# Kernel tuning notes

Measured on AMD Instinct MI355X. Metric: run time of the kernel, lower is better.

## Reference

```python
import jax, jax.numpy as jnp
import numpy as np

B, T, C = 2, 2048, 2048
H, KV, D = 16, 4, 128
G = H // KV  # kv groups
THETA = 10000.0


def setup_inputs() -> dict:
    key = jax.random.key(0)
    ks = jax.random.split(key, 5)
    x = jax.random.normal(ks[0], (B, T, C), dtype=jnp.float32)
    wq = jax.random.normal(ks[1], (H * D, C), dtype=jnp.float32) * 0.02
    wk = jax.random.normal(ks[2], (KV * D, C), dtype=jnp.float32) * 0.02
    wv = jax.random.normal(ks[3], (KV * D, C), dtype=jnp.float32) * 0.02
    wo = jax.random.normal(ks[4], (H * D, C), dtype=jnp.float32).T * 0.02  # [C, H*D] stored as [out,in]
    wo = jnp.asarray(wo)
    # rotary frequencies: freqs_cis = exp(i * t * theta^{-2j/D}) for j in [0, D/2)
    inv_freq = 1.0 / (THETA ** (jnp.arange(0, D, 2, dtype=jnp.float32) / D))  # [D/2]
    angles = jnp.arange(T, dtype=jnp.float32)[:, None] * inv_freq[None, :]    # [T, D/2]
    freqs_cos = jnp.cos(angles)
    freqs_sin = jnp.sin(angles)
    # additive causal mask [1,1,T,T]
    mask = jnp.where(jnp.tril(jnp.ones((T, T), dtype=bool)), 0.0, -1e9).astype(jnp.float32)[None, None]
    return {"x": x, "wq": wq, "wk": wk, "wv": wv, "wo": wo,
            "freqs_cos": freqs_cos, "freqs_sin": freqs_sin, "mask": mask}


def _apply_rope(t, cos, sin):
    # t: [B, T, nH, D]; cos/sin: [T, D/2]
    th = t.reshape(*t.shape[:-1], D // 2, 2)
    t0, t1 = th[..., 0], th[..., 1]
    c = cos[None, :, None, :]
    s = sin[None, :, None, :]
    o0 = t0 * c - t1 * s
    o1 = t0 * s + t1 * c
    return jnp.stack([o0, o1], axis=-1).reshape(t.shape)


def reference(x, wq, wk, wv, wo, freqs_cos, freqs_sin, mask):
    Bx, Tx, Cx = x.shape
    xq = (x @ wq.T).reshape(Bx, Tx, H, D)
    xk = (x @ wk.T).reshape(Bx, Tx, KV, D)
    xv = (x @ wv.T).reshape(Bx, Tx, KV, D)
    xq = _apply_rope(xq, freqs_cos, freqs_sin)
    xk = _apply_rope(xk, freqs_cos, freqs_sin)
    # GQA: repeat_interleave KV heads to match query heads
    xk = jnp.repeat(xk, G, axis=2)  # [B, T, H, D]
    xv = jnp.repeat(xv, G, axis=2)
    # [B, H, T, D]
    xq = xq.transpose(0, 2, 1, 3)
    xk = xk.transpose(0, 2, 1, 3)
    xv = xv.transpose(0, 2, 1, 3)
    scores = jnp.einsum('bhqd,bhkd->bhqk', xq, xk) / jnp.sqrt(jnp.float32(D))
    scores = scores + mask
    probs = jax.nn.softmax(scores.astype(jnp.float32), axis=-1).astype(xq.dtype)
    out = jnp.einsum('bhqk,bhkd->bhqd', probs, xv)
    out = out.transpose(0, 2, 1, 3).reshape(Bx, Tx, H * D)
    return out @ wo.T
```

## Files before the change

### kernel.cpp

```cpp
#include <hip/hip_runtime.h>
#include <hip/hip_bf16.h>

typedef __bf16 bf16_t;
typedef __bf16 bf16x8 __attribute__((ext_vector_type(8)));
typedef __bf16 bf16x4 __attribute__((ext_vector_type(4)));
typedef float f32x4 __attribute__((ext_vector_type(4)));
typedef float f32x16 __attribute__((ext_vector_type(16)));

#define SCALE_Q2 0.12752518895325724f

__device__ __forceinline__ void gload_lds16(const void* g, void* l) {
  __builtin_amdgcn_global_load_lds(
      (const __attribute__((address_space(1))) void*)g,
      (__attribute__((address_space(3))) void*)l, 16, 0, 0);
}

__global__ __launch_bounds__(256) void cvt_all(
    const float* __restrict__ x, const float* __restrict__ wq,
    const float* __restrict__ wk, const float* __restrict__ wv,
    const float* __restrict__ wo, bf16_t* __restrict__ xb,
    bf16_t* __restrict__ wqkv, bf16_t* __restrict__ wo_b) {
  int i = blockIdx.x * 256 + threadIdx.x;
  const int stride = gridDim.x * 256;
  for (; i < 4718592; i += stride) {
    const int e = i * 4;
    const float* src;
    bf16_t* dst;
    if (e < 8388608) {
      src = x + e;              dst = xb + e;
    } else if (e < 12582912) {
      src = wq + (e - 8388608); dst = wqkv + (e - 8388608);
    } else if (e < 13631488) {
      src = wk + (e - 12582912); dst = wqkv + (e - 8388608);
    } else if (e < 14680064) {
      src = wv + (e - 13631488); dst = wqkv + (e - 8388608);
    } else {
      src = wo + (e - 14680064); dst = wo_b + (e - 14680064);
    }
    f32x4 v = *reinterpret_cast<const f32x4*>(src);
    bf16x4 r;
    r[0] = (bf16_t)v[0]; r[1] = (bf16_t)v[1];
    r[2] = (bf16_t)v[2]; r[3] = (bf16_t)v[3];
    *reinterpret_cast<bf16x4*>(dst) = r;
  }
}

template <typename OutT>
__global__ __launch_bounds__(256) void gemm_bt(
    const bf16_t* __restrict__ A, const bf16_t* __restrict__ W,
    OutT* __restrict__ C, int M, int N, int K) {
  __shared__ __align__(16) bf16_t As[128 * 64];
  __shared__ __align__(16) bf16_t Ws[128 * 64];
  const int tid = threadIdx.x;
  const int lane = tid & 63;
  const int wid = tid >> 6;
  const int wr = wid >> 1, wc = wid & 1;
  const int l15 = lane & 15, lg = lane >> 4;
  const int r0 = blockIdx.y * 128;
  const int c0 = blockIdx.x * 128;

  f32x4 acc[4][4];
#pragma unroll
  for (int mi = 0; mi < 4; ++mi)
#pragma unroll
    for (int ni = 0; ni < 4; ++ni)
#pragma unroll
      for (int j = 0; j < 4; ++j) acc[mi][ni][j] = 0.f;

  for (int k0 = 0; k0 < K; k0 += 64) {
#pragma unroll
    for (int s = 0; s < 4; ++s) {
      const int c = s * 256 + tid;
      const int row = c >> 3;
      const int scol = (c & 7) ^ (row & 7);
      gload_lds16(A + (size_t)(r0 + row) * K + k0 + scol * 8,
                  (char*)As + c * 16);
      gload_lds16(W + (size_t)(c0 + row) * K + k0 + scol * 8,
                  (char*)Ws + c * 16);
    }
    __syncthreads();
#pragma unroll
    for (int kk = 0; kk < 2; ++kk) {
      bf16x8 af[4], wf[4];
#pragma unroll
      for (int mi = 0; mi < 4; ++mi) {
        const int r = wr * 64 + mi * 16 + l15;
        af[mi] = *reinterpret_cast<const bf16x8*>(
            (char*)As + r * 128 + ((kk * 64 + lg * 16) ^ ((r & 7) << 4)));
      }
#pragma unroll
      for (int ni = 0; ni < 4; ++ni) {
        const int r = wc * 64 + ni * 16 + l15;
        wf[ni] = *reinterpret_cast<const bf16x8*>(
            (char*)Ws + r * 128 + ((kk * 64 + lg * 16) ^ ((r & 7) << 4)));
      }
#pragma unroll
      for (int mi = 0; mi < 4; ++mi)
#pragma unroll
        for (int ni = 0; ni < 4; ++ni)
          acc[mi][ni] = __builtin_amdgcn_mfma_f32_16x16x32_bf16(
              af[mi], wf[ni], acc[mi][ni], 0, 0, 0);
    }
    __syncthreads();
  }

#pragma unroll
  for (int mi = 0; mi < 4; ++mi)
#pragma unroll
    for (int ni = 0; ni < 4; ++ni)
#pragma unroll
      for (int j = 0; j < 4; ++j) {
        const int row = r0 + wr * 64 + mi * 16 + lg * 4 + j;
        const int col = c0 + wc * 64 + ni * 16 + l15;
        const float v = acc[mi][ni][j];
        if constexpr (__is_same(OutT, float))
          C[(size_t)row * N + col] = v;
        else
          C[(size_t)row * N + col] = (bf16_t)v;
      }
}

__global__ __launch_bounds__(256) void rope_layout(
    const bf16_t* __restrict__ qkv, const float* __restrict__ fc,
    const float* __restrict__ fs, bf16_t* __restrict__ Qr,
    bf16_t* __restrict__ Kr) {
  const int n = blockIdx.x;
  const int b = n >> 11, t = n & 2047;
  const int tid = threadIdx.x;
  const bf16_t* row = qkv + (size_t)n * 3072;

#pragma unroll
  for (int i = 0; i < 4; ++i) {
    const int p = i * 256 + tid;
    const int h = p >> 6, j = p & 63;
    const float t0 = (float)row[h * 128 + 2 * j];
    const float t1 = (float)row[h * 128 + 2 * j + 1];
    const float c = fc[t * 64 + j], s = fs[t * 64 + j];
    const size_t dst = ((size_t)(b * 16 + h) * 2048 + t) * 128 + 2 * j;
    Qr[dst] = (bf16_t)((t0 * c - t1 * s) * SCALE_Q2);
    Qr[dst + 1] = (bf16_t)((t0 * s + t1 * c) * SCALE_Q2);
  }
  {
    const int kvh = tid >> 6, j = tid & 63;
    const float t0 = (float)row[2048 + kvh * 128 + 2 * j];
    const float t1 = (float)row[2048 + kvh * 128 + 2 * j + 1];
    const float c = fc[t * 64 + j], s = fs[t * 64 + j];
    const size_t dst = ((size_t)(b * 4 + kvh) * 2048 + t) * 128 + 2 * j;
    Kr[dst] = (bf16_t)(t0 * c - t1 * s);
    Kr[dst + 1] = (bf16_t)(t0 * s + t1 * c);
  }
}

__global__ __launch_bounds__(256) void v_trans(
    const bf16_t* __restrict__ qkv, bf16_t* __restrict__ Vt) {
  __shared__ bf16_t L[64][68];
  const int bid = blockIdx.x;
  const int tt = bid & 31;
  const int dt2 = (bid >> 5) & 1;
  const int bk = bid >> 6;
  const int b = bk >> 2, kvh = bk & 3;
  const int t0 = tt * 64, d0 = dt2 * 64;
  const int r = threadIdx.x >> 4;
  const int c4 = (threadIdx.x & 15) * 4;

#pragma unroll
  for (int it = 0; it < 4; ++it) {
    const int tl = r + it * 16;
    const int tp = (tl & ~15) |
                   ((tl & 3) | ((tl & 4) << 1) | ((tl & 8) >> 1));
    const bf16_t* src = qkv + (size_t)(b * 2048 + t0 + tl) * 3072 + 2560 +
                        kvh * 128 + d0 + c4;
    *reinterpret_cast<bf16x4*>(&L[tp][c4]) =
        *reinterpret_cast<const bf16x4*>(src);
  }
  __syncthreads();
#pragma unroll
  for (int it = 0; it < 4; ++it) {
    const int dr = r + it * 16;
    bf16x4 v;
#pragma unroll
    for (int j = 0; j < 4; ++j) v[j] = L[c4 + j][dr];
    *reinterpret_cast<bf16x4*>(Vt + ((size_t)bk * 128 + d0 + dr) * 2048 +
                               t0 + c4) = v;
  }
}

#define VLOAD(buf, kf, kc)                                               \
  {                                                                      \
    _Pragma("unroll") for (int dtile_ = 0; dtile_ < 4; ++dtile_)         \
        buf[dtile_] = *reinterpret_cast<const bf16x8*>(                  \
            Vbase + (size_t)(dtile_ * 32 + l31) * 2048 + k0 + (kf) * 32 +\
            (kc) * 16 + hi * 8);                                         \
  }

__global__ __launch_bounds__(256, 2) void attn_fwd(
    const bf16_t* __restrict__ Qr, const bf16_t* __restrict__ Kr,
    const bf16_t* __restrict__ Vt, bf16_t* __restrict__ Oout) {
  __shared__ __align__(16) bf16_t Klds[2][128 * 128];
  const int tid = threadIdx.x;
  const int lane = tid & 63, w = tid >> 6;
  const int l31 = lane & 31, hi = lane >> 5;
  const int sidx = blockIdx.x >> 5;
  const int hb = blockIdx.x & 31;
  const int h = hb & 15, b = hb >> 4;
  const int kvh = h >> 2;
  const int st = (sidx < 8) ? (15 - sidx) : (sidx - 8);

  const bf16_t* Kbase = Kr + ((size_t)(b * 4 + kvh) * 2048) * 128;
  const bf16_t* Vbase = Vt + ((size_t)(b * 4 + kvh) * 128) * 2048;

  const int qbw = st * 128 + w * 32;
  const bf16_t* Qbase = Qr + ((size_t)(b * 16 + h) * 2048 + qbw + l31) * 128;

  auto STAGE = [&](bf16_t* dst, int kt) {
    const int k0s = kt * 128;
#pragma unroll
    for (int i = 0; i < 8; ++i) {
      const int c = i * 256 + tid;
      const int row = c >> 4;
      const int col = c & 15;
      const int scol = col ^ (row & 15);
      gload_lds16(Kbase + (size_t)(k0s + row) * 128 + scol * 8, dst + c * 8);
    }
  };

  STAGE(&Klds[0][0], 0);

  bf16x8 qf[8];
#pragma unroll
  for (int dt = 0; dt < 8; ++dt)
    qf[dt] = *reinterpret_cast<const bf16x8*>(Qbase + dt * 16 + hi * 8);

  f32x16 o[4];
#pragma unroll
  for (int d = 0; d < 4; ++d)
#pragma unroll
    for (int r = 0; r < 16; ++r) o[d][r] = 0.f;
  float lsum = 0.f;

  const int nt = st + 1;
  int cur = 0;
  for (int kt = 0; kt < nt; ++kt) {
    const int k0 = kt * 128;
    const bool last = (kt == nt - 1);
    const int kfmax = last ? w : 3;

    __syncthreads();
    if (kt + 1 < nt) STAGE(&Klds[cur ^ 1][0], kt + 1);

    const char* KB = (const char*)&Klds[cur][0];

    bf16x8 vaA[4], vaB[4];
    VLOAD(vaA, 0, 0);
    VLOAD(vaB, 0, 1);

#pragma unroll
    for (int kp = 0; kp < 2; ++kp) {
      f32x16 sA, sB;
      __builtin_amdgcn_s_setprio(1);
      if (2 * kp <= kfmax) {
#pragma unroll
        for (int r = 0; r < 16; ++r) sA[r] = 0.f;
#pragma unroll
        for (int dt = 0; dt < 8; ++dt) {
          const int boff = ((2 * kp) * 32 + l31) * 256 +
                           ((dt * 32 + hi * 16) ^ ((l31 & 15) << 4));
          bf16x8 ka = *reinterpret_cast<const bf16x8*>(KB + boff);
          sA = __builtin_amdgcn_mfma_f32_32x32x16_bf16(ka, qf[dt], sA, 0, 0, 0);
        }
      }
      if (2 * kp + 1 <= kfmax) {
#pragma unroll
        for (int r = 0; r < 16; ++r) sB[r] = 0.f;
#pragma unroll
        for (int dt = 0; dt < 8; ++dt) {
          const int boff = ((2 * kp + 1) * 32 + l31) * 256 +
                           ((dt * 32 + hi * 16) ^ ((l31 & 15) << 4));
          bf16x8 ka = *reinterpret_cast<const bf16x8*>(KB + boff);
          sB = __builtin_amdgcn_mfma_f32_32x32x16_bf16(ka, qf[dt], sB, 0, 0, 0);
        }
      }
      __builtin_amdgcn_s_setprio(0);

#pragma unroll
      for (int ki = 0; ki < 2; ++ki) {
        const int kf = 2 * kp + ki;
        if (kf <= kfmax) {
          const bool diag = last && (kf == w);
          float p[16];
#pragma unroll
          for (int r = 0; r < 16; ++r) {
            float e = exp2f(ki ? sB[r] : sA[r]);
            if (diag) {
              const int crow = (r & 3) + 8 * (r >> 2) + 4 * hi;
              if (crow > l31) e = 0.f;
            }
            p[r] = e;
          }
          const float t0 = (p[0] + p[1]) + (p[2] + p[3]);
          const float t1 = (p[4] + p[5]) + (p[6] + p[7]);
          const float t2 = (p[8] + p[9]) + (p[10] + p[11]);
          const float t3 = (p[12] + p[13]) + (p[14] + p[15]);
          lsum += (t0 + t1) + (t2 + t3);

          {
            unsigned int u0, u1, u2, u3;
            asm("v_cvt_pk_bf16_f32 %0, %1, %2" : "=v"(u0)
                : "v"(p[0]), "v"(p[1]));
            asm("v_cvt_pk_bf16_f32 %0, %1, %2" : "=v"(u1)
                : "v"(p[2]), "v"(p[3]));
            asm("v_cvt_pk_bf16_f32 %0, %1, %2" : "=v"(u2)
                : "v"(p[4]), "v"(p[5]));
            asm("v_cvt_pk_bf16_f32 %0, %1, %2" : "=v"(u3)
                : "v"(p[6]), "v"(p[7]));
            union { unsigned int u[4]; bf16x8 v; } pb;
            pb.u[0] = u0; pb.u[1] = u1; pb.u[2] = u2; pb.u[3] = u3;
            __builtin_amdgcn_s_setprio(1);
#pragma unroll
            for (int dtile = 0; dtile < 4; ++dtile)
              o[dtile] = __builtin_amdgcn_mfma_f32_32x32x16_bf16(
                  vaA[dtile], pb.v, o[dtile], 0, 0, 0);
            __builtin_amdgcn_s_setprio(0);
          }
          if (kf < kfmax) VLOAD(vaA, kf + 1, 0);

          {
            unsigned int u0, u1, u2, u3;
            asm("v_cvt_pk_bf16_f32 %0, %1, %2" : "=v"(u0)
                : "v"(p[8]), "v"(p[9]));
            asm("v_cvt_pk_bf16_f32 %0, %1, %2" : "=v"(u1)
                : "v"(p[10]), "v"(p[11]));
            asm("v_cvt_pk_bf16_f32 %0, %1, %2" : "=v"(u2)
                : "v"(p[12]), "v"(p[13]));
            asm("v_cvt_pk_bf16_f32 %0, %1, %2" : "=v"(u3)
                : "v"(p[14]), "v"(p[15]));
            union { unsigned int u[4]; bf16x8 v; } pb;
            pb.u[0] = u0; pb.u[1] = u1; pb.u[2] = u2; pb.u[3] = u3;
            __builtin_amdgcn_s_setprio(1);
#pragma unroll
            for (int dtile = 0; dtile < 4; ++dtile)
              o[dtile] = __builtin_amdgcn_mfma_f32_32x32x16_bf16(
                  vaB[dtile], pb.v, o[dtile], 0, 0, 0);
            __builtin_amdgcn_s_setprio(0);
          }
          if (kf < kfmax) VLOAD(vaB, kf + 1, 1);
        }
      }
    }
    cur ^= 1;
  }

  const float ltot = lsum + __shfl_xor(lsum, 32);
  const float inv = 1.f / ltot;
  bf16_t* Obase = Oout + ((size_t)b * 2048 + qbw + l31) * 2048 + h * 128;
#pragma unroll
  for (int dtile = 0; dtile < 4; ++dtile)
#pragma unroll
    for (int g = 0; g < 4; ++g) {
      bf16x4 stv;
#pragma unroll
      for (int j = 0; j < 4; ++j)
        stv[j] = (bf16_t)(o[dtile][g * 4 + j] * inv);
      *reinterpret_cast<bf16x4*>(Obase + dtile * 32 + 8 * g + 4 * hi) = stv;
    }
}

extern "C" void kernel_launch(void* const* d_in, const int* in_sizes, int n_in,
                              void* d_out, int out_size, void* d_ws,
                              size_t ws_size, hipStream_t stream) {
  const float* x  = (const float*)d_in[0];
  const float* wq = (const float*)d_in[1];
  const float* wk = (const float*)d_in[2];
  const float* wv = (const float*)d_in[3];
  const float* wo = (const float*)d_in[4];
  const float* fc = (const float*)d_in[5];
  const float* fs = (const float*)d_in[6];
  float* out = (float*)d_out;

  char* ws = (char*)d_ws;
  bf16_t* xb      = (bf16_t*)(ws + 0);
  bf16_t* wqkv    = (bf16_t*)(ws + 16777216);
  bf16_t* wo_b    = (bf16_t*)(ws + 29360128);
  bf16_t* qkv     = (bf16_t*)(ws + 37748736);
  bf16_t* Qr      = (bf16_t*)(ws + 62914560);
  bf16_t* Kr      = (bf16_t*)(ws + 79691776);
  bf16_t* Vt      = (bf16_t*)(ws + 83886080);
  bf16_t* attn_o  = xb;

  const int M = 4096;

  cvt_all<<<2048, 256, 0, stream>>>(x, wq, wk, wv, wo, xb, wqkv, wo_b);

  gemm_bt<bf16_t><<<dim3(3072 / 128, M / 128), 256, 0, stream>>>(
      xb, wqkv, qkv, M, 3072, 2048);

  rope_layout<<<4096, 256, 0, stream>>>(qkv, fc, fs, Qr, Kr);
  v_trans<<<512, 256, 0, stream>>>(qkv, Vt);

  attn_fwd<<<512, 256, 0, stream>>>(Qr, Kr, Vt, attn_o);

  gemm_bt<float><<<dim3(2048 / 128, M / 128), 256, 0, stream>>>(
      attn_o, wo_b, out, M, 2048, 2048);
}
```

Measured before the change: 213.1 us.

## Double-buffer GEMM LDS, fuse rope with V transpose, compute row sums via MFMA

The GEMM now double-buffers its LDS tiles. It issues the next tile's global-to-LDS loads before computing on the current tile, which removes one barrier per iteration. The rope and V-transpose kernels are merged into a single launch to save launch overhead. The attention kernel now computes the softmax denominator with an extra MFMA against a ones vector instead of VALU adds and a cross-lane shuffle. This adds MFMA work, and doubling the GEMM's LDS use may lower occupancy.

Measured after the change: 217.3 us. No clear change (+2.0%).

```diff
diff --git a/kernel.cpp b/kernel.cpp
--- a/kernel.cpp
+++ b/kernel.cpp
@@ -49,8 +49,8 @@
 __global__ __launch_bounds__(256) void gemm_bt(
     const bf16_t* __restrict__ A, const bf16_t* __restrict__ W,
     OutT* __restrict__ C, int M, int N, int K) {
-  __shared__ __align__(16) bf16_t As[128 * 64];
-  __shared__ __align__(16) bf16_t Ws[128 * 64];
+  __shared__ __align__(16) bf16_t As[2][128 * 64];
+  __shared__ __align__(16) bf16_t Ws[2][128 * 64];
   const int tid = threadIdx.x;
   const int lane = tid & 63;
   const int wid = tid >> 6;
@@ -67,18 +67,25 @@
 #pragma unroll
       for (int j = 0; j < 4; ++j) acc[mi][ni][j] = 0.f;
 
-  for (int k0 = 0; k0 < K; k0 += 64) {
+  auto STAGE = [&](int buf, int k0) {
 #pragma unroll
     for (int s = 0; s < 4; ++s) {
       const int c = s * 256 + tid;
       const int row = c >> 3;
       const int scol = (c & 7) ^ (row & 7);
       gload_lds16(A + (size_t)(r0 + row) * K + k0 + scol * 8,
-                  (char*)As + c * 16);
+                  (char*)As[buf] + c * 16);
       gload_lds16(W + (size_t)(c0 + row) * K + k0 + scol * 8,
-                  (char*)Ws + c * 16);
-    }
+                  (char*)Ws[buf] + c * 16);
+    }
+  };
+
+  const int nt = K >> 6;
+  STAGE(0, 0);
+  int cur = 0;
+  for (int t = 0; t < nt; ++t) {
     __syncthreads();
+    if (t + 1 < nt) STAGE(cur ^ 1, (t + 1) * 64);
 #pragma unroll
     for (int kk = 0; kk < 2; ++kk) {
       bf16x8 af[4], wf[4];
@@ -86,13 +93,13 @@
       for (int mi = 0; mi < 4; ++mi) {
         const int r = wr * 64 + mi * 16 + l15;
         af[mi] = *reinterpret_cast<const bf16x8*>(
-            (char*)As + r * 128 + ((kk * 64 + lg * 16) ^ ((r & 7) << 4)));
+            (char*)As[cur] + r * 128 + ((kk * 64 + lg * 16) ^ ((r & 7) << 4)));
       }
 #pragma unroll
       for (int ni = 0; ni < 4; ++ni) {
         const int r = wc * 64 + ni * 16 + l15;
         wf[ni] = *reinterpret_cast<const bf16x8*>(
-            (char*)Ws + r * 128 + ((kk * 64 + lg * 16) ^ ((r & 7) << 4)));
+            (char*)Ws[cur] + r * 128 + ((kk * 64 + lg * 16) ^ ((r & 7) << 4)));
       }
 #pragma unroll
       for (int mi = 0; mi < 4; ++mi)
@@ -101,7 +108,7 @@
           acc[mi][ni] = __builtin_amdgcn_mfma_f32_16x16x32_bf16(
               af[mi], wf[ni], acc[mi][ni], 0, 0, 0);
     }
-    __syncthreads();
+    cur ^= 1;
   }
 
 #pragma unroll
@@ -120,68 +127,65 @@
       }
 }
 
-__global__ __launch_bounds__(256) void rope_layout(
+__global__ __launch_bounds__(256) void rope_vtrans(
     const bf16_t* __restrict__ qkv, const float* __restrict__ fc,
     const float* __restrict__ fs, bf16_t* __restrict__ Qr,
-    bf16_t* __restrict__ Kr) {
-  const int n = blockIdx.x;
-  const int b = n >> 11, t = n & 2047;
+    bf16_t* __restrict__ Kr, bf16_t* __restrict__ Vt) {
+  __shared__ bf16_t L[64][68];
   const int tid = threadIdx.x;
-  const bf16_t* row = qkv + (size_t)n * 3072;
-
-#pragma unroll
-  for (int i = 0; i < 4; ++i) {
-    const int p = i * 256 + tid;
-    const int h = p >> 6, j = p & 63;
-    const float t0 = (float)row[h * 128 + 2 * j];
-    const float t1 = (float)row[h * 128 + 2 * j + 1];
-    const float c = fc[t * 64 + j], s = fs[t * 64 + j];
-    const size_t dst = ((size_t)(b * 16 + h) * 2048 + t) * 128 + 2 * j;
-    Qr[dst] = (bf16_t)((t0 * c - t1 * s) * SCALE_Q2);
-    Qr[dst + 1] = (bf16_t)((t0 * s + t1 * c) * SCALE_Q2);
-  }
-  {
-    const int kvh = tid >> 6, j = tid & 63;
-    const float t0 = (float)row[2048 + kvh * 128 + 2 * j];
-    const float t1 = (float)row[2048 + kvh * 128 + 2 * j + 1];
-    const float c = fc[t * 64 + j], s = fs[t * 64 + j];
-    const size_t dst = ((size_t)(b * 4 + kvh) * 2048 + t) * 128 + 2 * j;
-    Kr[dst] = (bf16_t)(t0 * c - t1 * s);
-    Kr[dst + 1] = (bf16_t)(t0 * s + t1 * c);
-  }
-}
-
-__global__ __launch_bounds__(256) void v_trans(
-    const bf16_t* __restrict__ qkv, bf16_t* __restrict__ Vt) {
-  __shared__ bf16_t L[64][68];
-  const int bid = blockIdx.x;
-  const int tt = bid & 31;
-  const int dt2 = (bid >> 5) & 1;
-  const int bk = bid >> 6;
-  const int b = bk >> 2, kvh = bk & 3;
-  const int t0 = tt * 64, d0 = dt2 * 64;
-  const int r = threadIdx.x >> 4;
-  const int c4 = (threadIdx.x & 15) * 4;
-
-#pragma unroll
-  for (int it = 0; it < 4; ++it) {
-    const int tl = r + it * 16;
-    const int tp = (tl & ~15) |
-                   ((tl & 3) | ((tl & 4) << 1) | ((tl & 8) >> 1));
-    const bf16_t* src = qkv + (size_t)(b * 2048 + t0 + tl) * 3072 + 2560 +
-                        kvh * 128 + d0 + c4;
-    *reinterpret_cast<bf16x4*>(&L[tp][c4]) =
-        *reinterpret_cast<const bf16x4*>(src);
-  }
-  __syncthreads();
-#pragma unroll
-  for (int it = 0; it < 4; ++it) {
-    const int dr = r + it * 16;
-    bf16x4 v;
-#pragma unroll
-    for (int j = 0; j < 4; ++j) v[j] = L[c4 + j][dr];
-    *reinterpret_cast<bf16x4*>(Vt + ((size_t)bk * 128 + d0 + dr) * 2048 +
-                               t0 + c4) = v;
+  if (blockIdx.x < 4096) {
+    const int n = blockIdx.x;
+    const int b = n >> 11, t = n & 2047;
+    const bf16_t* row = qkv + (size_t)n * 3072;
+#pragma unroll
+    for (int i = 0; i < 4; ++i) {
+      const int p = i * 256 + tid;
+      const int h = p >> 6, j = p & 63;
+      const float t0 = (float)row[h * 128 + 2 * j];
+      const float t1 = (float)row[h * 128 + 2 * j + 1];
+      const float c = fc[t * 64 + j], s = fs[t * 64 + j];
+      const size_t dst = ((size_t)(b * 16 + h) * 2048 + t) * 128 + 2 * j;
+      Qr[dst] = (bf16_t)((t0 * c - t1 * s) * SCALE_Q2);
+      Qr[dst + 1] = (bf16_t)((t0 * s + t1 * c) * SCALE_Q2);
+    }
+    {
+      const int kvh = tid >> 6, j = tid & 63;
+      const float t0 = (float)row[2048 + kvh * 128 + 2 * j];
+      const float t1 = (float)row[2048 + kvh * 128 + 2 * j + 1];
+      const float c = fc[t * 64 + j], s = fs[t * 64 + j];
+      const size_t dst = ((size_t)(b * 4 + kvh) * 2048 + t) * 128 + 2 * j;
+      Kr[dst] = (bf16_t)(t0 * c - t1 * s);
+      Kr[dst + 1] = (bf16_t)(t0 * s + t1 * c);
+    }
+  } else {
+    const int bid = blockIdx.x - 4096;
+    const int tt = bid & 31;
+    const int dt2 = (bid >> 5) & 1;
+    const int bk = bid >> 6;
+    const int b = bk >> 2, kvh = bk & 3;
+    const int t0 = tt * 64, d0 = dt2 * 64;
+    const int r = tid >> 4;
+    const int c4 = (tid & 15) * 4;
+#pragma unroll
+    for (int it = 0; it < 4; ++it) {
+      const int tl = r + it * 16;
+      const int tp = (tl & ~15) |
+                     ((tl & 3) | ((tl & 4) << 1) | ((tl & 8) >> 1));
+      const bf16_t* src = qkv + (size_t)(b * 2048 + t0 + tl) * 3072 + 2560 +
+                          kvh * 128 + d0 + c4;
+      *reinterpret_cast<bf16x4*>(&L[tp][c4]) =
+          *reinterpret_cast<const bf16x4*>(src);
+    }
+    __syncthreads();
+#pragma unroll
+    for (int it = 0; it < 4; ++it) {
+      const int dr = r + it * 16;
+      bf16x4 v;
+#pragma unroll
+      for (int j = 0; j < 4; ++j) v[j] = L[c4 + j][dr];
+      *reinterpret_cast<bf16x4*>(Vt + ((size_t)bk * 128 + d0 + dr) * 2048 +
+                                 t0 + c4) = v;
+    }
   }
 }
 
@@ -231,12 +235,18 @@
   for (int dt = 0; dt < 8; ++dt)
     qf[dt] = *reinterpret_cast<const bf16x8*>(Qbase + dt * 16 + hi * 8);
 
+  bf16x8 onesv;
+#pragma unroll
+  for (int i = 0; i < 8; ++i) onesv[i] = (bf16_t)1.0f;
+
   f32x16 o[4];
 #pragma unroll
   for (int d = 0; d < 4; ++d)
 #pragma unroll
     for (int r = 0; r < 16; ++r) o[d][r] = 0.f;
-  float lsum = 0.f;
+  f32x16 osum;
+#pragma unroll
+  for (int r = 0; r < 16; ++r) osum[r] = 0.f;
 
   const int nt = st + 1;
   int cur = 0;
@@ -297,11 +307,6 @@
             }
             p[r] = e;
           }
-          const float t0 = (p[0] + p[1]) + (p[2] + p[3]);
-          const float t1 = (p[4] + p[5]) + (p[6] + p[7]);
-          const float t2 = (p[8] + p[9]) + (p[10] + p[11]);
-          const float t3 = (p[12] + p[13]) + (p[14] + p[15]);
-          lsum += (t0 + t1) + (t2 + t3);
 
           {
             unsigned int u0, u1, u2, u3;
@@ -316,6 +321,8 @@
             union { unsigned int u[4]; bf16x8 v; } pb;
             pb.u[0] = u0; pb.u[1] = u1; pb.u[2] = u2; pb.u[3] = u3;
             __builtin_amdgcn_s_setprio(1);
+            osum = __builtin_amdgcn_mfma_f32_32x32x16_bf16(onesv, pb.v, osum,
+                                                           0, 0, 0);
 #pragma unroll
             for (int dtile = 0; dtile < 4; ++dtile)
               o[dtile] = __builtin_amdgcn_mfma_f32_32x32x16_bf16(
@@ -337,6 +344,8 @@
             union { unsigned int u[4]; bf16x8 v; } pb;
             pb.u[0] = u0; pb.u[1] = u1; pb.u[2] = u2; pb.u[3] = u3;
             __builtin_amdgcn_s_setprio(1);
+            osum = __builtin_amdgcn_mfma_f32_32x32x16_bf16(onesv, pb.v, osum,
+                                                           0, 0, 0);
 #pragma unroll
             for (int dtile = 0; dtile < 4; ++dtile)
               o[dtile] = __builtin_amdgcn_mfma_f32_32x32x16_bf16(
@@ -350,8 +359,7 @@
     cur ^= 1;
   }
 
-  const float ltot = lsum + __shfl_xor(lsum, 32);
-  const float inv = 1.f / ltot;
+  const float inv = 1.f / osum[0];
   bf16_t* Obase = Oout + ((size_t)b * 2048 + qbw + l31) * 2048 + h * 128;
 #pragma unroll
   for (int dtile = 0; dtile < 4; ++dtile)
@@ -394,8 +402,7 @@
   gemm_bt<bf16_t><<<dim3(3072 / 128, M / 128), 256, 0, stream>>>(
       xb, wqkv, qkv, M, 3072, 2048);
 
-  rope_layout<<<4096, 256, 0, stream>>>(qkv, fc, fs, Qr, Kr);
-  v_trans<<<512, 256, 0, stream>>>(qkv, Vt);
+  rope_vtrans<<<4608, 256, 0, stream>>>(qkv, fc, fs, Qr, Kr, Vt);
 
   attn_fwd<<<512, 256, 0, stream>>>(Qr, Kr, Vt, attn_o);
 
```
